# Kernel optimization log

Hardware: AMD Instinct MI355X
Metric: run time of the kernel (lower is better)

The kernel has to match this reference:

```python
import jax, jax.numpy as jnp
import numpy as np

NH = 12  # num_heads


def _rms(y, g, eps=1e-6):
    # RMSNorm over the full model dim (applied before the head reshape, as in the source)
    return y * jax.lax.rsqrt(jnp.mean(y * y, axis=-1, keepdims=True) + eps) * g


def _rope(t, cos, sin, total_len):
    # t: [B, S, n, d]; rotate first total_len tokens, pass the tail through unchanged
    b, s, n, d = t.shape
    c = d // 2
    tm = t[:, :total_len].reshape(b, total_len, n, c, 2)
    tr, ti = tm[..., 0], tm[..., 1]
    co = cos[None, :, None, :]
    si = sin[None, :, None, :]
    rot = jnp.stack([tr * co - ti * si, tr * si + ti * co], axis=-1).reshape(b, total_len, n, d)
    if total_len < s:
        return jnp.concatenate([rot, t[:, total_len:]], axis=1)
    return rot


def setup_inputs() -> dict:
    key = jax.random.key(0)
    ks = jax.random.split(key, 8)
    B, F, H, W = 4, 4, 16, 28
    S = F * H * W  # 1792 tokens
    D = 1536
    d = D // NH    # 128
    c = d // 2     # 64
    MAXSEQ = 64
    x = jax.random.normal(ks[0], (B, S, D), jnp.float32)
    seq_lens = jnp.full((B,), S, dtype=jnp.int32)
    grid_sizes = jnp.tile(jnp.array([[F, H, W]], dtype=jnp.int32), (B, 1))
    ang = jnp.arange(MAXSEQ, dtype=jnp.float32)[:, None] * (
        10000.0 ** (-jnp.arange(c, dtype=jnp.float32) / c))[None, :]
    w = lambda k, shp: jax.random.normal(k, shp, jnp.float32) * 0.02
    return {
        "x": x,
        "seq_lens": seq_lens,
        "grid_sizes": grid_sizes,
        "freqs_cos": jnp.cos(ang),
        "freqs_sin": jnp.sin(ang),
        "Wq": w(ks[1], (D, D)), "bq": jnp.zeros((D,), jnp.float32),
        "Wk": w(ks[2], (D, D)), "bk": jnp.zeros((D,), jnp.float32),
        "Wv": w(ks[3], (D, D)), "bv": jnp.zeros((D,), jnp.float32),
        "Wo": w(ks[4], (D, D)), "bo": jnp.zeros((D,), jnp.float32),
        "gq": jnp.ones((D,), jnp.float32),
        "gk": jnp.ones((D,), jnp.float32),
        "num_modalities": 1,
    }


def reference(x, seq_lens, grid_sizes, freqs_cos, freqs_sin,
              Wq, bq, Wk, bk, Wv, bv, Wo, bo, gq, gk, num_modalities):
    b, s, D = x.shape
    d = D // NH
    c = d // 2
    # QKV projections + RMSNorm on q/k (norm over the full dim, then split heads)
    q = _rms(x @ Wq.T + bq, gq).reshape(b, s, NH, d)
    k = _rms(x @ Wk.T + bk, gk).reshape(b, s, NH, d)
    v = (x @ Wv.T + bv).reshape(b, s, NH, d)
    # grid metadata is static (same grid for all samples in this setup)
    f, h, w = (int(z) for z in np.asarray(grid_sizes)[0])
    m = int(num_modalities)
    ct = c - 2 * (c // 3)
    ch = c // 3
    seq_per = f * h * w
    total_len = min(seq_per * m, s)

    def grid_freqs(fr):
        # build per-token (t,h,w) frequency table: [seq_per, c], tiled over modalities
        ft = jnp.broadcast_to(fr[:f, :ct][:, None, None, :], (f, h, w, ct))
        fh = jnp.broadcast_to(fr[:h, ct:ct + ch][None, :, None, :], (f, h, w, ch))
        fw = jnp.broadcast_to(fr[:w, ct + ch:c][None, None, :, :], (f, h, w, ch))
        base = jnp.concatenate([ft, fh, fw], axis=-1).reshape(seq_per, c)
        return jnp.tile(base, (m, 1))[:total_len]

    cos = grid_freqs(freqs_cos)
    sin = grid_freqs(freqs_sin)
    q = _rope(q, cos, sin, total_len)
    k = _rope(k, cos, sin, total_len)
    # full (window_size=(-1,-1)) attention with k_lens masking
    scale = 1.0 / jnp.sqrt(jnp.float32(d))
    scores = jnp.einsum('bqhd,bkhd->bhqk', q, k) * scale
    kmask = jnp.arange(s)[None, :] < seq_lens[:, None]  # [B, S]
    scores = jnp.where(kmask[:, None, None, :], scores, jnp.float32(-1e30))
    attn = jax.nn.softmax(scores, axis=-1)
    out = jnp.einsum('bhqk,bkhd->bqhd', attn, v).reshape(b, s, D)
    return out @ Wo.T + bo
```

## Files before the change

### kernel.cpp

```cpp
#include <hip/hip_runtime.h>
#include <hip/hip_bf16.h>

typedef short bf16x8 __attribute__((ext_vector_type(8)));
typedef float f32x4 __attribute__((ext_vector_type(4)));
typedef float f32x16 __attribute__((ext_vector_type(16)));

#define NH 12
#define SEQ 1792
#define DMODEL 1536
#define HD 128

static __device__ __forceinline__ void gload16(const void* g, void* l) {
  __builtin_amdgcn_global_load_lds((const __attribute__((address_space(1))) void*)g,
                                   (__attribute__((address_space(3))) void*)l, 16, 0, 0);
}

static __device__ __forceinline__ short f2bf(float x) {
  __hip_bfloat16 h = __float2bfloat16(x);
  return *reinterpret_cast<short*>(&h);
}

static __device__ __forceinline__ unsigned pack2(float lo, float hi) {
  unsigned a = (unsigned)(unsigned short)f2bf(lo);
  unsigned b = (unsigned)(unsigned short)f2bf(hi);
  return a | (b << 16);
}

__global__ __launch_bounds__(256) void cast_all_kernel(
    const float* __restrict__ x, const float* __restrict__ wq, const float* __restrict__ wk,
    const float* __restrict__ wv, const float* __restrict__ wo,
    __hip_bfloat16* __restrict__ xb, __hip_bfloat16* __restrict__ wb,
    __hip_bfloat16* __restrict__ wob) {
  int i = blockIdx.x * 256 + threadIdx.x;
  const float* src; __hip_bfloat16* dst; int j;
  if (i < 2752512)      { src = x;  dst = xb;            j = i; }
  else if (i < 3342336) { src = wq; dst = wb;            j = i - 2752512; }
  else if (i < 3932160) { src = wk; dst = wb + 2359296;  j = i - 3342336; }
  else if (i < 4521984) { src = wv; dst = wb + 4718592;  j = i - 3932160; }
  else if (i < 5111808) { src = wo; dst = wob;           j = i - 4521984; }
  else return;
  float4 v = reinterpret_cast<const float4*>(src)[j];
  short4 r;
  r.x = f2bf(v.x); r.y = f2bf(v.y); r.z = f2bf(v.z); r.w = f2bf(v.w);
  reinterpret_cast<short4*>(dst)[j] = r;
}

template<int MODE>
__global__ __launch_bounds__(512, 2) void gemm8(
    const __hip_bfloat16* __restrict__ A, const __hip_bfloat16* __restrict__ B,
    int nN, int cpx,
    const float* __restrict__ bq, const float* __restrict__ bk, const float* __restrict__ bv,
    __hip_bfloat16* __restrict__ qbuf, __hip_bfloat16* __restrict__ kbuf,
    __hip_bfloat16* __restrict__ vt,
    const float* __restrict__ bo, float* __restrict__ outp)
{
  constexpr int K = DMODEL;
  constexpr int nT = K / 64;
  constexpr int nIt = nT / 2;
  __shared__ char LDSRAW[131072];
  const int tid = threadIdx.x;
  const int l = tid & 63, w = tid >> 6;
  const int lr = l & 15, lg = l >> 4;
  const int wr = w >> 2, wc = w & 3;

  const int orig = blockIdx.x;
  const int wg = (orig & 7) * cpx + (orig >> 3);
  const int m0 = (wg / nN) * 256, n0 = (wg % nN) * 256;

  const int hrow0 = tid >> 3;
  const int scb0 = ((tid & 7) << 4) ^ ((hrow0 & 7) << 4);

  auto stageA = [&](int t, int half) {
    const char* s = (const char*)(A + (size_t)(m0 + half * 128) * K + t * 64);
    char* d = LDSRAW + (t & 1) * 32768 + half * 16384;
    gload16(s + (size_t)hrow0 * (K * 2) + scb0, d + tid * 16);
    gload16(s + (size_t)(hrow0 + 64) * (K * 2) + scb0, d + (tid + 512) * 16);
  };
  auto stageB = [&](int t, int half) {
    const char* s = (const char*)(B + (size_t)(n0 + half * 128) * K + t * 64);
    char* d = LDSRAW + 65536 + (t & 1) * 32768 + half * 16384;
    gload16(s + (size_t)hrow0 * (K * 2) + scb0, d + tid * 16);
    gload16(s + (size_t)(hrow0 + 64) * (K * 2) + scb0, d + (tid + 512) * 16);
  };

  f32x4 acc[8][4] = {};
  bf16x8 afr0[4][2], afr1[4][2], b0e[2][2], b0o[2][2], b1f[2][2];

  auto RA = [&](int p, int mh, bf16x8 (&dst)[4][2]) {
    const char* base = LDSRAW + p * 32768 + wr * 16384;
#pragma unroll
    for (int i = 0; i < 4; ++i) {
      int hrow = (mh * 4 + i) * 16 + lr;
#pragma unroll
      for (int ks = 0; ks < 2; ++ks)
        dst[i][ks] = *reinterpret_cast<const bf16x8*>(
            base + hrow * 128 + ((ks * 64 + lg * 16) ^ ((hrow & 7) << 4)));
    }
  };
  auto RB = [&](int p, int nh, bf16x8 (&dst)[2][2]) {
#pragma unroll
    for (int j = 0; j < 2; ++j) {
      int cbase = wc * 64 + (nh * 2 + j) * 16;
      int half = cbase >> 7;
      int hrow = (cbase & 127) + lr;
      const char* base = LDSRAW + 65536 + p * 32768 + half * 16384;
#pragma unroll
      for (int ks = 0; ks < 2; ++ks)
        dst[j][ks] = *reinterpret_cast<const bf16x8*>(
            base + hrow * 128 + ((ks * 64 + lg * 16) ^ ((hrow & 7) << 4)));
    }
  };
  auto MF = [&](int mh, int nh, bf16x8 (&a)[4][2], bf16x8 (&b)[2][2]) {
    __builtin_amdgcn_s_setprio(1);
#pragma unroll
    for (int i = 0; i < 4; ++i)
#pragma unroll
      for (int j = 0; j < 2; ++j)
#pragma unroll
        for (int ks = 0; ks < 2; ++ks)
          acc[mh * 4 + i][nh * 2 + j] = __builtin_amdgcn_mfma_f32_16x16x32_bf16(
              a[i][ks], b[j][ks], acc[mh * 4 + i][nh * 2 + j], 0, 0, 0);
    __builtin_amdgcn_s_setprio(0);
  };

#define SB0 __builtin_amdgcn_sched_barrier(0)
#define BAR __builtin_amdgcn_s_barrier()
#define TILE(p, t, b0c, b0n)                                                 \
  { RB(p, 1, b1f);                                                           \
    if ((t) + 1 < nT) stageA((t) + 1, 1);                                    \
    SB0;                                                                     \
    MF(0, 0, afr0, b0c);                                                     \
    BAR;                                                                     \
    RA(p, 1, afr1);                                                          \
    if ((t) + 1 < nT) stageB((t) + 1, 0);                                    \
    SB0;                                                                     \
    MF(0, 1, afr0, b1f);                                                     \
    BAR;                                                                     \
    if ((t) + 1 < nT) stageB((t) + 1, 1);                                    \
    if ((t) + 2 < nT) stageA((t) + 2, 0);                                    \
    SB0;                                                                     \
    MF(1, 1, afr1, b1f);                                                     \
    if ((t) + 2 < nT) asm volatile("s_waitcnt vmcnt(2)" ::: "memory");       \
    else              asm volatile("s_waitcnt vmcnt(0)" ::: "memory");       \
    BAR;                                                                     \
    if ((t) + 1 < nT) { RA((p) ^ 1, 0, afr0); RB((p) ^ 1, 0, b0n); }         \
    SB0;                                                                     \
    MF(1, 0, afr1, b0c);                                                     \
    BAR;                                                                     \
  }

  stageA(0, 0); stageA(0, 1); stageB(0, 0); stageB(0, 1); stageA(1, 0);
  asm volatile("s_waitcnt vmcnt(2)" ::: "memory");
  BAR;
  RA(0, 0, afr0); RB(0, 0, b0e);

  for (int it2 = 0; it2 < nIt; ++it2) {
    TILE(0, 2 * it2, b0e, b0o);
    TILE(1, 2 * it2 + 1, b0o, b0e);
  }
#undef TILE
#undef SB0
#undef BAR

  if (MODE == 0) {
    const int which = n0 / DMODEL;
    if (which < 2) {
#pragma unroll
      for (int fj = 0; fj < 4; ++fj) {
        int ncol = n0 + wc * 64 + fj * 16 + lr;
        int cc = ncol - which * DMODEL;
        int hh = cc >> 7, dd = cc & 127;
        float bias = (which == 0 ? bq : bk)[cc];
#pragma unroll
        for (int fi = 0; fi < 8; ++fi)
#pragma unroll
          for (int r = 0; r < 4; ++r) {
            int rowg = m0 + wr * 128 + fi * 16 + lg * 4 + r;
            int bbb = rowg / SEQ;
            int sr = rowg - bbb * SEQ;
            __hip_bfloat16 hv = __float2bfloat16(acc[fi][fj][r] + bias);
            if (which == 0)
              qbuf[(((size_t)(bbb * NH + hh)) * SEQ + sr) * HD + dd] = hv;
            else
              kbuf[(((size_t)(bbb * NH + hh)) * SEQ + sr) * HD + dd] = hv;
          }
      }
    } else {
      __syncthreads();
      const int cc0 = n0 - 2 * DMODEL;
#pragma unroll
      for (int fj = 0; fj < 4; ++fj) {
        int d_loc = wc * 64 + fj * 16 + lr;
        float bias = bv[cc0 + d_loc];
#pragma unroll
        for (int fi = 0; fi < 8; ++fi)
#pragma unroll
          for (int r = 0; r < 4; ++r) {
            int s_loc = wr * 128 + fi * 16 + lg * 4 + r;
            *reinterpret_cast<short*>(LDSRAW + d_loc * 512 +
                ((s_loc * 2) ^ ((d_loc & 7) << 4))) = f2bf(acc[fi][fj][r] + bias);
          }
      }
      __syncthreads();
      const int bbb = m0 / SEQ;
      const int sr0 = m0 - bbb * SEQ;
#pragma unroll
      for (int c = 0; c < 16; ++c) {
        int g = c * 512 + tid;
        int d = g >> 5;
        int sb = (g & 31) << 4;
        bf16x8 vvv = *reinterpret_cast<const bf16x8*>(
            LDSRAW + d * 512 + (sb ^ ((d & 7) << 4)));
        int ddg = cc0 + d, hh = ddg >> 7, dd = ddg & 127;
        *reinterpret_cast<bf16x8*>(
            &vt[(((size_t)(bbb * NH + hh)) * HD + dd) * SEQ + sr0 + (sb >> 1)]) = vvv;
      }
    }
  } else {
#pragma unroll
    for (int fj = 0; fj < 4; ++fj) {
      int ncol = n0 + wc * 64 + fj * 16 + lr;
      float bias = bo[ncol];
#pragma unroll
      for (int fi = 0; fi < 8; ++fi)
#pragma unroll
        for (int r = 0; r < 4; ++r) {
          int rowg = m0 + wr * 128 + fi * 16 + lg * 4 + r;
          outp[(size_t)rowg * DMODEL + ncol] = acc[fi][fj][r] + bias;
        }
    }
  }
}

__global__ __launch_bounds__(256) void rmsrope_kernel(
    __hip_bfloat16* __restrict__ qb, __hip_bfloat16* __restrict__ kb,
    const float* __restrict__ gq, const float* __restrict__ gk,
    const float* __restrict__ fc, const float* __restrict__ fs,
    const int* __restrict__ gsz, const int* __restrict__ nmod)
{
  const int bs = blockIdx.x;
  const int b = bs / SEQ, s = bs - b * SEQ;
  const int t = threadIdx.x;
  const int f = gsz[0], h = gsz[1], wd = gsz[2];
  const int mm = nmod[0];
  const int seq_per = f * h * wd;
  int total_len = seq_per * mm; if (total_len > SEQ) total_len = SEQ;
  const bool dorope = s < total_len;
  int fi = 0, hi2 = 0, wi = 0;
  if (dorope) {
    int p = s % seq_per;
    fi = p / (h * wd);
    int rem = p - fi * (h * wd);
    hi2 = rem / wd;
    wi = rem - hi2 * wd;
  }
  float qv[3][2], kv[3][2];
  float sq = 0.f, sk = 0.f;
#pragma unroll
  for (int r = 0; r < 3; ++r) {
    int pi = t + r * 256;
    int head = pi >> 6;
    int dd = (pi & 63) * 2;
    size_t addr = (((size_t)(b * NH + head)) * SEQ + s) * HD + dd;
    __hip_bfloat162 q2 = *reinterpret_cast<const __hip_bfloat162*>(&qb[addr]);
    __hip_bfloat162 k2 = *reinterpret_cast<const __hip_bfloat162*>(&kb[addr]);
    qv[r][0] = __bfloat162float(q2.x); qv[r][1] = __bfloat162float(q2.y);
    kv[r][0] = __bfloat162float(k2.x); kv[r][1] = __bfloat162float(k2.y);
    sq += qv[r][0] * qv[r][0] + qv[r][1] * qv[r][1];
    sk += kv[r][0] * kv[r][0] + kv[r][1] * kv[r][1];
  }
#pragma unroll
  for (int off = 1; off < 64; off <<= 1) {
    sq += __shfl_xor(sq, off);
    sk += __shfl_xor(sk, off);
  }
  __shared__ float red[2][4];
  if ((t & 63) == 0) { red[0][t >> 6] = sq; red[1][t >> 6] = sk; }
  __syncthreads();
  float tq = red[0][0] + red[0][1] + red[0][2] + red[0][3];
  float tk = red[1][0] + red[1][1] + red[1][2] + red[1][3];
  float rq = rsqrtf(tq * (1.0f / DMODEL) + 1e-6f);
  float rk = rsqrtf(tk * (1.0f / DMODEL) + 1e-6f);
  const float scale = 0.08838834764831845f;
#pragma unroll
  for (int r = 0; r < 3; ++r) {
    int pi = t + r * 256;
    int head = pi >> 6;
    int dd = (pi & 63) * 2;
    int col = pi * 2;
    size_t addr = (((size_t)(b * NH + head)) * SEQ + s) * HD + dd;
    float q0 = qv[r][0] * rq * gq[col], q1 = qv[r][1] * rq * gq[col + 1];
    float k0 = kv[r][0] * rk * gk[col], k1 = kv[r][1] * rk * gk[col + 1];
    if (dorope) {
      int j = pi & 63;
      int row = (j < 22) ? fi : (j < 43) ? hi2 : wi;
      float co = fc[row * 64 + j], si = fs[row * 64 + j];
      float a;
      a = q0 * co - q1 * si; q1 = q0 * si + q1 * co; q0 = a;
      a = k0 * co - k1 * si; k1 = k0 * si + k1 * co; k0 = a;
    }
    q0 *= scale; q1 *= scale;
    __hip_bfloat162 oq, ok;
    oq.x = __float2bfloat16(q0); oq.y = __float2bfloat16(q1);
    ok.x = __float2bfloat16(k0); ok.y = __float2bfloat16(k1);
    *reinterpret_cast<__hip_bfloat162*>(&qb[addr]) = oq;
    *reinterpret_cast<__hip_bfloat162*>(&kb[addr]) = ok;
  }
}

__global__ __launch_bounds__(256, 2) void attn_kernel(
    const __hip_bfloat16* __restrict__ qb, const __hip_bfloat16* __restrict__ kbuf,
    const __hip_bfloat16* __restrict__ vt, const int* __restrict__ seq_lens,
    __hip_bfloat16* __restrict__ ob)
{
  const int orig = blockIdx.x;
  const int wg = (orig & 7) * 84 + (orig >> 3);
  const int bh = wg / 14, qt = wg % 14;
  const int bbb = bh / NH, hh = bh - bbb * NH;
  const int tid = threadIdx.x;
  const int w = tid >> 6, l = tid & 63;
  const int lq = l & 31, h = l >> 5;
  const int sl = seq_lens[bbb];
  const __hip_bfloat16* Q = qb + (size_t)bh * SEQ * HD;
  const char* Kc = (const char*)(kbuf + (size_t)bh * SEQ * HD);
  const __hip_bfloat16* Vp = vt + (size_t)bh * HD * SEQ;
  const int q0 = qt * 128 + w * 32;

  __shared__ __hip_bfloat16 Kt[2][64 * 128];
  __shared__ __hip_bfloat16 Vt[128 * 64];

  bf16x8 qf[8];
#pragma unroll
  for (int kc = 0; kc < 8; ++kc)
    qf[kc] = *reinterpret_cast<const bf16x8*>(
        &Q[(size_t)(q0 + lq) * HD + kc * 16 + h * 8]);

  f32x16 oacc[4] = {};
  float m = -3e38f, ll = 0.f;

  const int nkt = (sl + 63) >> 6;

  auto stageK = [&](int buf, int k0) {
    char* Lb = (char*)&Kt[buf][0];
#pragma unroll
    for (int q2 = 0; q2 < 4; ++q2) {
      int chunk = q2 * 256 + tid;
      int row = chunk >> 4;
      int cb = (chunk & 15) << 4;
      int scb = cb ^ ((row & 7) << 4);
      gload16(Kc + (size_t)(k0 + row) * 256 + scb, Lb + chunk * 16);
    }
  };
  auto stageV = [&](int k0) {
    char* Lb = (char*)&Vt[0];
#pragma unroll
    for (int q2 = 0; q2 < 4; ++q2) {
      int chunk = q2 * 256 + tid;
      int row = chunk >> 3;
      int cb = (chunk & 7) << 4;
      int scb = cb ^ ((row & 7) << 4);
      gload16(Vp + (size_t)row * SEQ + k0 + (scb >> 1), Lb + chunk * 16);
    }
  };

  stageK(0, 0);
  for (int kt = 0; kt < nkt; ++kt) {
    __syncthreads();
    const int k0 = kt * 64;
    stageV(k0);
    const bool pf = (kt + 1 < nkt);
    if (pf) stageK((kt + 1) & 1, k0 + 64);
    const char* Kl = (const char*)&Kt[kt & 1][0];
    const char* Vl = (const char*)&Vt[0];

    f32x16 sa[2] = {};
    __builtin_amdgcn_s_setprio(1);
#pragma unroll
    for (int cb = 0; cb < 2; ++cb) {
      int row = cb * 32 + lq;
      int swz = (row & 7) << 4;
#pragma unroll
      for (int kc = 0; kc < 8; ++kc) {
        bf16x8 kf = *reinterpret_cast<const bf16x8*>(
            Kl + row * 256 + ((kc * 32 + h * 16) ^ swz));
        sa[cb] = __builtin_amdgcn_mfma_f32_32x32x16_bf16(kf, qf[kc], sa[cb], 0, 0, 0);
      }
    }
    __builtin_amdgcn_s_setprio(0);

    if (k0 + 64 > sl) {
#pragma unroll
      for (int cb = 0; cb < 2; ++cb)
#pragma unroll
        for (int r = 0; r < 16; ++r) {
          int kg = k0 + cb * 32 + (r & 3) + 8 * (r >> 2) + 4 * h;
          if (kg >= sl) sa[cb][r] = -3e38f;
        }
    }

    float mx = -3e38f;
#pragma unroll
    for (int cb = 0; cb < 2; ++cb)
#pragma unroll
      for (int r = 0; r < 16; ++r) mx = fmaxf(mx, sa[cb][r]);
    mx = fmaxf(mx, __shfl_xor(mx, 32));

    if (__any(mx - m > 8.f)) {
      float mn = fmaxf(m, mx);
      float alpha = __expf(m - mn);
      m = mn;
      ll *= alpha;
#pragma unroll
      for (int r = 0; r < 16; ++r) {
        float ar = __shfl(alpha, (r & 3) + 8 * (r >> 2) + 4 * h);
#pragma unroll
        for (int d0 = 0; d0 < 4; ++d0) oacc[d0][r] *= ar;
      }
    }

    float rs = 0.f;
#pragma unroll
    for (int cb = 0; cb < 2; ++cb)
#pragma unroll
      for (int r = 0; r < 16; ++r) {
        float e = __expf(sa[cb][r] - m);
        sa[cb][r] = e;
        rs += e;
      }
    rs += __shfl_xor(rs, 32);
    ll += rs;

    bf16x8 pa[4];
#pragma unroll
    for (int c = 0; c < 4; ++c) {
      const int cb = c >> 1, r0 = 8 * (c & 1);
      unsigned A01 = pack2(sa[cb][r0],     sa[cb][r0 + 1]);
      unsigned A23 = pack2(sa[cb][r0 + 2], sa[cb][r0 + 3]);
      unsigned B01 = pack2(sa[cb][r0 + 4], sa[cb][r0 + 5]);
      unsigned B23 = pack2(sa[cb][r0 + 6], sa[cb][r0 + 7]);
      unsigned s1 = __shfl_xor(h ? A01 : B01, 32);
      unsigned s2 = __shfl_xor(h ? A23 : B23, 32);
      int4 wv;
      wv.x = (int)(h ? s1 : A01);
      wv.y = (int)(h ? s2 : A23);
      wv.z = (int)(h ? B01 : s1);
      wv.w = (int)(h ? B23 : s2);
      pa[c] = *reinterpret_cast<bf16x8*>(&wv);
    }

    if (pf) asm volatile("s_waitcnt vmcnt(4)" ::: "memory");
    else    asm volatile("s_waitcnt vmcnt(0)" ::: "memory");
    __builtin_amdgcn_s_barrier();

    __builtin_amdgcn_s_setprio(1);
#pragma unroll
    for (int c = 0; c < 4; ++c)
#pragma unroll
      for (int d0 = 0; d0 < 4; ++d0) {
        int vr = d0 * 32 + lq;
        bf16x8 vv = *reinterpret_cast<const bf16x8*>(
            Vl + vr * 128 + ((c * 32 + h * 16) ^ ((vr & 7) << 4)));
        oacc[d0] = __builtin_amdgcn_mfma_f32_32x32x16_bf16(pa[c], vv, oacc[d0], 0, 0, 0);
      }
    __builtin_amdgcn_s_setprio(0);
  }

  float invl = 1.0f / ll;
#pragma unroll
  for (int r = 0; r < 16; ++r) {
    int qoff = (r & 3) + 8 * (r >> 2) + 4 * h;
    float ir = __shfl(invl, qoff);
    int qrow = q0 + qoff;
#pragma unroll
    for (int d0 = 0; d0 < 4; ++d0)
      ob[((size_t)bbb * SEQ + qrow) * DMODEL + hh * HD + d0 * 32 + lq] =
          __float2bfloat16(oacc[d0][r] * ir);
  }
}

extern "C" void kernel_launch(void* const* d_in, const int* in_sizes, int n_in,
                              void* d_out, int out_size, void* d_ws, size_t ws_size,
                              hipStream_t stream) {
  const float* x   = (const float*)d_in[0];
  const int* seq_lens   = (const int*)d_in[1];
  const int* grid_sizes = (const int*)d_in[2];
  const float* fc  = (const float*)d_in[3];
  const float* fs  = (const float*)d_in[4];
  const float* Wq  = (const float*)d_in[5];
  const float* bq  = (const float*)d_in[6];
  const float* Wk  = (const float*)d_in[7];
  const float* bk  = (const float*)d_in[8];
  const float* Wv  = (const float*)d_in[9];
  const float* bv  = (const float*)d_in[10];
  const float* Wo  = (const float*)d_in[11];
  const float* bo  = (const float*)d_in[12];
  const float* gq  = (const float*)d_in[13];
  const float* gk  = (const float*)d_in[14];
  const int* nmod  = (const int*)d_in[15];
  float* out = (float*)d_out;

  char* ws = (char*)d_ws;
  __hip_bfloat16* xb   = (__hip_bfloat16*)(ws + 0);
  __hip_bfloat16* wb   = (__hip_bfloat16*)(ws + 22020096);
  __hip_bfloat16* wob  = (__hip_bfloat16*)(ws + 36175872);
  __hip_bfloat16* qbuf = (__hip_bfloat16*)(ws + 40894464);
  __hip_bfloat16* kbuf = (__hip_bfloat16*)(ws + 62914560);
  __hip_bfloat16* vtb  = (__hip_bfloat16*)(ws + 84934656);
  __hip_bfloat16* ob   = xb;

  cast_all_kernel<<<(5111808 + 255) / 256, 256, 0, stream>>>(x, Wq, Wk, Wv, Wo, xb, wb, wob);

  gemm8<0><<<504, 512, 0, stream>>>(xb, wb, 18, 63, bq, bk, bv,
                                    qbuf, kbuf, vtb, nullptr, nullptr);
  rmsrope_kernel<<<7168, 256, 0, stream>>>(qbuf, kbuf, gq, gk, fc, fs, grid_sizes, nmod);
  attn_kernel<<<672, 256, 0, stream>>>(qbuf, kbuf, vtb, seq_lens, ob);
  gemm8<1><<<168, 512, 0, stream>>>(ob, wob, 6, 21, nullptr, nullptr, nullptr,
                                    nullptr, nullptr, nullptr, bo, out);
}
```

Measured before the change: 325.4 us.

## Stage Q/K GEMM epilogue through LDS and remap workgroups to 2D chunks

The Q/K branch of the QKV GEMM epilogue now writes its bias-added bf16 tile into swizzled LDS and then emits 16-byte vector stores to the head-major q/k buffers. Before, it wrote scattered 2-byte global stores. The workgroup-to-tile mapping also changes from a linear chunk per XCD (blockIdx & 7) to 2D chunks of 7 M-tiles by nNc N-tiles, so that each XCD's L2 sees a compact block of A and B rows. The costs are an extra LDS round trip with two barriers in the epilogue, and a swizzle that now depends on the grid shape (7 M-tiles per chunk).

After: 345.5 us. 1.06x slower.

```diff
diff --git a/kernel.cpp b/kernel.cpp
--- a/kernel.cpp
+++ b/kernel.cpp
@@ -48,7 +48,7 @@
 template<int MODE>
 __global__ __launch_bounds__(512, 2) void gemm8(
     const __hip_bfloat16* __restrict__ A, const __hip_bfloat16* __restrict__ B,
-    int nN, int cpx,
+    int nN, int nNc,
     const float* __restrict__ bq, const float* __restrict__ bk, const float* __restrict__ bv,
     __hip_bfloat16* __restrict__ qbuf, __hip_bfloat16* __restrict__ kbuf,
     __hip_bfloat16* __restrict__ vt,
@@ -64,8 +64,11 @@
   const int wr = w >> 2, wc = w & 3;
 
   const int orig = blockIdx.x;
-  const int wg = (orig & 7) * cpx + (orig >> 3);
-  const int m0 = (wg / nN) * 256, n0 = (wg % nN) * 256;
+  const int cx = orig & 7, i = orig >> 3;
+  const int chunks_n = nN / nNc;
+  const int cm = cx / chunks_n, cn = cx - cm * chunks_n;
+  const int mi = i % 7, ni = i / 7;
+  const int m0 = (cm * 7 + mi) * 256, n0 = (cn * nNc + ni) * 256;
 
   const int hrow0 = tid >> 3;
   const int scb0 = ((tid & 7) << 4) ^ ((hrow0 & 7) << 4);
@@ -89,11 +92,11 @@
   auto RA = [&](int p, int mh, bf16x8 (&dst)[4][2]) {
     const char* base = LDSRAW + p * 32768 + wr * 16384;
 #pragma unroll
-    for (int i = 0; i < 4; ++i) {
-      int hrow = (mh * 4 + i) * 16 + lr;
+    for (int ii = 0; ii < 4; ++ii) {
+      int hrow = (mh * 4 + ii) * 16 + lr;
 #pragma unroll
       for (int ks = 0; ks < 2; ++ks)
-        dst[i][ks] = *reinterpret_cast<const bf16x8*>(
+        dst[ii][ks] = *reinterpret_cast<const bf16x8*>(
             base + hrow * 128 + ((ks * 64 + lg * 16) ^ ((hrow & 7) << 4)));
     }
   };
@@ -113,13 +116,13 @@
   auto MF = [&](int mh, int nh, bf16x8 (&a)[4][2], bf16x8 (&b)[2][2]) {
     __builtin_amdgcn_s_setprio(1);
 #pragma unroll
-    for (int i = 0; i < 4; ++i)
+    for (int ii = 0; ii < 4; ++ii)
 #pragma unroll
       for (int j = 0; j < 2; ++j)
 #pragma unroll
         for (int ks = 0; ks < 2; ++ks)
-          acc[mh * 4 + i][nh * 2 + j] = __builtin_amdgcn_mfma_f32_16x16x32_bf16(
-              a[i][ks], b[j][ks], acc[mh * 4 + i][nh * 2 + j], 0, 0, 0);
+          acc[mh * 4 + ii][nh * 2 + j] = __builtin_amdgcn_mfma_f32_16x16x32_bf16(
+              a[ii][ks], b[j][ks], acc[mh * 4 + ii][nh * 2 + j], 0, 0, 0);
     __builtin_amdgcn_s_setprio(0);
   };
 
@@ -164,26 +167,37 @@
 
   if (MODE == 0) {
     const int which = n0 / DMODEL;
+    const int bbb = m0 / SEQ;
+    const int sr0 = m0 - bbb * SEQ;
     if (which < 2) {
+      __syncthreads();
+      const int cc0 = n0 - which * DMODEL;
 #pragma unroll
       for (int fj = 0; fj < 4; ++fj) {
-        int ncol = n0 + wc * 64 + fj * 16 + lr;
-        int cc = ncol - which * DMODEL;
-        int hh = cc >> 7, dd = cc & 127;
-        float bias = (which == 0 ? bq : bk)[cc];
+        int d_loc = wc * 64 + fj * 16 + lr;
+        float bias = (which == 0 ? bq : bk)[cc0 + d_loc];
 #pragma unroll
         for (int fi = 0; fi < 8; ++fi)
 #pragma unroll
           for (int r = 0; r < 4; ++r) {
-            int rowg = m0 + wr * 128 + fi * 16 + lg * 4 + r;
-            int bbb = rowg / SEQ;
-            int sr = rowg - bbb * SEQ;
-            __hip_bfloat16 hv = __float2bfloat16(acc[fi][fj][r] + bias);
-            if (which == 0)
-              qbuf[(((size_t)(bbb * NH + hh)) * SEQ + sr) * HD + dd] = hv;
-            else
-              kbuf[(((size_t)(bbb * NH + hh)) * SEQ + sr) * HD + dd] = hv;
+            int s_loc = wr * 128 + fi * 16 + lg * 4 + r;
+            *reinterpret_cast<short*>(LDSRAW + s_loc * 512 +
+                ((d_loc * 2) ^ ((s_loc & 7) << 4))) = f2bf(acc[fi][fj][r] + bias);
           }
+      }
+      __syncthreads();
+      __hip_bfloat16* dst = (which == 0 ? qbuf : kbuf);
+#pragma unroll
+      for (int c = 0; c < 16; ++c) {
+        int g = c * 512 + tid;
+        int s = g >> 5;
+        int db = (g & 31) << 4;
+        bf16x8 q8 = *reinterpret_cast<const bf16x8*>(
+            LDSRAW + s * 512 + (db ^ ((s & 7) << 4)));
+        int d = cc0 + (db >> 1);
+        int hh = d >> 7, dd = d & 127;
+        *reinterpret_cast<bf16x8*>(
+            &dst[(((size_t)(bbb * NH + hh)) * SEQ + sr0 + s) * HD + dd]) = q8;
       }
     } else {
       __syncthreads();
@@ -202,8 +216,6 @@
           }
       }
       __syncthreads();
-      const int bbb = m0 / SEQ;
-      const int sr0 = m0 - bbb * SEQ;
 #pragma unroll
       for (int c = 0; c < 16; ++c) {
         int g = c * 512 + tid;
@@ -510,10 +522,10 @@
 
   cast_all_kernel<<<(5111808 + 255) / 256, 256, 0, stream>>>(x, Wq, Wk, Wv, Wo, xb, wb, wob);
 
-  gemm8<0><<<504, 512, 0, stream>>>(xb, wb, 18, 63, bq, bk, bv,
+  gemm8<0><<<504, 512, 0, stream>>>(xb, wb, 18, 9, bq, bk, bv,
                                     qbuf, kbuf, vtb, nullptr, nullptr);
   rmsrope_kernel<<<7168, 256, 0, stream>>>(qbuf, kbuf, gq, gk, fc, fs, grid_sizes, nmod);
   attn_kernel<<<672, 256, 0, stream>>>(qbuf, kbuf, vtb, seq_lens, ob);
-  gemm8<1><<<168, 512, 0, stream>>>(ob, wob, 6, 21, nullptr, nullptr, nullptr,
+  gemm8<1><<<168, 512, 0, stream>>>(ob, wob, 6, 3, nullptr, nullptr, nullptr,
                                     nullptr, nullptr, nullptr, bo, out);
 }
```
